# Kernel optimization log

Hardware: AMD Instinct MI355X
Metric: run time of the kernel (lower is better)

## Reference

```python
import jax, jax.numpy as jnp
import numpy as np

K_MASK = -2.3819763e38  # gemma masking constant


def apply_rope(inputs, positions, head_dim):
    # inputs: [B, T, N, H], positions: [B, T]
    half = head_dim // 2
    fraction = 2.0 * jnp.arange(half, dtype=jnp.float32) / head_dim
    timescale = 10000.0 ** fraction                      # [half]
    sinusoid = positions[..., None].astype(jnp.float32) / timescale  # [B, T, half]
    sin = jnp.sin(sinusoid)[:, :, None, :]               # [B, T, 1, half]
    cos = jnp.cos(sinusoid)[:, :, None, :]
    first, second = jnp.split(inputs, 2, axis=-1)
    out = jnp.concatenate([first * cos - second * sin,
                           second * cos + first * sin], axis=-1)
    return out.astype(inputs.dtype)


def setup_inputs() -> dict:
    key = jax.random.key(0)
    k0, k1, k2, k3 = jax.random.split(key, 4)
    B, T, D, N, H = 4, 1024, 2048, 16, 128
    x = jax.random.normal(k0, (B, T, D), dtype=jnp.float32)
    wq = jax.random.normal(k1, (N, D, H), dtype=jnp.float32) * 0.02
    wkv = jax.random.normal(k2, (2, 1, D, H), dtype=jnp.float32) * 0.02  # MQA: 1 kv head
    wo = jax.random.normal(k3, (N, H, D), dtype=jnp.float32) * 0.02
    segment_pos = jnp.broadcast_to(jnp.arange(T, dtype=jnp.int32), (B, T))
    attn_mask = jnp.broadcast_to(jnp.tril(jnp.ones((T, T), dtype=bool)), (B, T, T))
    return {"x": x, "wq": wq, "wkv": wkv, "wo": wo,
            "segment_pos": segment_pos, "attn_mask": attn_mask}


def reference(x, wq, wkv, wo, segment_pos, attn_mask):
    N, _, H = wq.shape
    # projections
    q = jnp.einsum('BTD,NDH->BTNH', x, wq)          # [B,T,N,H]
    kv = jnp.einsum('BSD,CKDH->CBSKH', x, wkv)      # [2,B,S,1,H]
    k, v = kv[0], kv[1]
    # RoPE + scaling
    q = apply_rope(q, segment_pos, H) * (H ** -0.5)
    k = apply_rope(k, segment_pos, H)
    # MQA head repeat: 1 kv head -> N heads
    k = jnp.repeat(k, N, axis=-2)                   # [B,S,N,H]
    v = jnp.repeat(v, N, axis=-2)
    # attention with manual masked softmax
    logits = jnp.einsum('BTNH,BSNH->BTNS', q, k)
    padded = jnp.where(attn_mask[:, :, None, :], logits, K_MASK)
    probs = jax.nn.softmax(padded, axis=-1).astype(k.dtype)
    encoded = jnp.einsum('BTNS,BSNH->BTNH', probs, v)
    return jnp.einsum('BTNH,NHD->BTD', encoded, wo)
```

## Files before the change

kernel.cpp:

```cpp
#include <hip/hip_runtime.h>
#include <cstdint>
#include <cstddef>

typedef unsigned short u16;
typedef __attribute__((ext_vector_type(8))) short bf16x8;
typedef __attribute__((ext_vector_type(4))) float f32x4;

#define B_ 4
#define T_ 1024
#define D_ 2048
#define N_ 16
#define H_ 128
#define BT_ (B_ * T_)
#define KMASK (-2.3819763e38f)

__device__ __forceinline__ u16 f2bf(float f) {
  uint32_t u = __builtin_bit_cast(uint32_t, f);
  u += 0x7FFFu + ((u >> 16) & 1u);
  return (u16)(u >> 16);
}
__device__ __forceinline__ float bf2f(uint32_t u) {
  return __builtin_bit_cast(float, u << 16);
}

__device__ __forceinline__ void gload16(const void* g, void* l) {
  __builtin_amdgcn_global_load_lds((const __attribute__((address_space(1))) void*)g,
                                   (__attribute__((address_space(3))) void*)l, 16, 0, 0);
}

__global__ __launch_bounds__(256) void convert_x_kernel(const float* __restrict__ x,
                                                        u16* __restrict__ xb) {
  int i = (blockIdx.x * 256 + threadIdx.x) * 8;
  float4 v0 = *(const float4*)(x + i);
  float4 v1 = *(const float4*)(x + i + 4);
  uint4 o;
  o.x = (uint32_t)f2bf(v0.x) | ((uint32_t)f2bf(v0.y) << 16);
  o.y = (uint32_t)f2bf(v0.z) | ((uint32_t)f2bf(v0.w) << 16);
  o.z = (uint32_t)f2bf(v1.x) | ((uint32_t)f2bf(v1.y) << 16);
  o.w = (uint32_t)f2bf(v1.z) | ((uint32_t)f2bf(v1.w) << 16);
  *(uint4*)(xb + i) = o;
}

__global__ __launch_bounds__(256) void transpose_kernel(const float* __restrict__ src,
                                                        u16* __restrict__ dst, int R, int C) {
  __shared__ float tile[32][33];
  const int z = blockIdx.z;
  const float* s = src + (size_t)z * R * C;
  u16* d = dst + (size_t)z * R * C;
  const int tx = threadIdx.x, ty = threadIdx.y;
  const int r0 = blockIdx.y * 32, c0 = blockIdx.x * 32;
#pragma unroll
  for (int i = 0; i < 4; ++i)
    tile[ty + i * 8][tx] = s[(size_t)(r0 + ty + i * 8) * C + (c0 + tx)];
  __syncthreads();
#pragma unroll
  for (int i = 0; i < 4; ++i)
    d[(size_t)(c0 + ty + i * 8) * R + (r0 + tx)] = f2bf(tile[tx][ty + i * 8]);
}

__global__ __launch_bounds__(256) void rope_table_kernel(float* __restrict__ costab,
                                                         float* __restrict__ sintab) {
  int idx = blockIdx.x * 256 + threadIdx.x;
  int p = idx >> 6, i = idx & 63;
  float ts = powf(10000.0f, (float)i * (1.0f / 64.0f));
  float ang = (float)p / ts;
  costab[idx] = cosf(ang);
  sintab[idx] = sinf(ang);
}

__global__ __launch_bounds__(256) void proj_gemm_kernel(
    const u16* __restrict__ xb, const u16* __restrict__ wqT, const u16* __restrict__ wkvT,
    u16* __restrict__ qraw, u16* __restrict__ kraw, u16* __restrict__ vT) {
  __shared__ alignas(16) u16 a_lds[128 * 64];
  __shared__ alignas(16) u16 b_lds[128 * 64];
  const int bid = blockIdx.x;
  const int newbid = (bid & 7) * 72 + (bid >> 3);
  const int y = newbid >> 5;
  const int m0 = (newbid & 31) * 128;
  const u16* Bt = (y < N_) ? (wqT + (size_t)y * H_ * D_) : (wkvT + (size_t)(y - N_) * H_ * D_);
  const int tid = threadIdx.x;
  const int w = tid >> 6, lane = tid & 63;
  const int g = lane >> 4, li = lane & 15;
  const int mrow = (w >> 1) * 64, wc = (w & 1) * 64;
  f32x4 acc[4][4];
#pragma unroll
  for (int i = 0; i < 4; ++i)
#pragma unroll
    for (int j = 0; j < 4; ++j) acc[i][j] = (f32x4){0.f, 0.f, 0.f, 0.f};

  for (int k0 = 0; k0 < D_; k0 += 64) {
    __syncthreads();
#pragma unroll
    for (int it = 0; it < 4; ++it) {
      int chunk = it * 256 + tid;
      int row = chunk >> 3, cu = chunk & 7;
      gload16(xb + (size_t)(m0 + row) * D_ + k0 + ((cu ^ (row & 7)) << 3), &a_lds[chunk * 8]);
    }
#pragma unroll
    for (int it = 0; it < 4; ++it) {
      int chunk = it * 256 + tid;
      int row = chunk >> 3, cu = chunk & 7;
      gload16(Bt + (size_t)row * D_ + k0 + ((cu ^ (row & 7)) << 3), &b_lds[chunk * 8]);
    }
    __syncthreads();
#pragma unroll
    for (int c2 = 0; c2 < 2; ++c2) {
      bf16x8 af[4], bfr[4];
#pragma unroll
      for (int i = 0; i < 4; ++i) {
        int row = mrow + i * 16 + li;
        af[i] = *(const bf16x8*)((const char*)a_lds +
                                 row * 128 + ((c2 * 64 + g * 16) ^ ((row & 7) << 4)));
      }
#pragma unroll
      for (int j = 0; j < 4; ++j) {
        int row = wc + j * 16 + li;
        bfr[j] = *(const bf16x8*)((const char*)b_lds +
                                  row * 128 + ((c2 * 64 + g * 16) ^ ((row & 7) << 4)));
      }
#pragma unroll
      for (int i = 0; i < 4; ++i)
#pragma unroll
        for (int j = 0; j < 4; ++j)
          acc[i][j] = __builtin_amdgcn_mfma_f32_16x16x32_bf16(af[i], bfr[j], acc[i][j], 0, 0, 0);
    }
  }

  const int b = m0 >> 10;
  if (y == N_ + 1) {
    const int tbase0 = (m0 & 1023) + mrow;
#pragma unroll
    for (int i = 0; i < 4; ++i) {
      int tbase = tbase0 + i * 16 + g * 4;
#pragma unroll
      for (int j = 0; j < 4; ++j) {
        int h = wc + j * 16 + li;
        ushort4 pk;
        pk.x = f2bf(acc[i][j][0]);
        pk.y = f2bf(acc[i][j][1]);
        pk.z = f2bf(acc[i][j][2]);
        pk.w = f2bf(acc[i][j][3]);
        *(ushort4*)(vT + ((size_t)(b * H_ + h)) * T_ + tbase) = pk;
      }
    }
  } else {
    size_t rowbase = (y < N_) ? ((size_t)(b * N_ + y) * T_ + (m0 & 1023)) : (size_t)m0;
    u16* dst0 = (y < N_) ? qraw : kraw;
#pragma unroll
    for (int i = 0; i < 4; ++i)
#pragma unroll
      for (int r = 0; r < 4; ++r) {
        int trow = mrow + i * 16 + g * 4 + r;
        u16* dst = dst0 + (rowbase + trow) * H_;
#pragma unroll
        for (int j = 0; j < 4; ++j) dst[wc + j * 16 + li] = f2bf(acc[i][j][r]);
      }
  }
}

__global__ __launch_bounds__(256) void rope_apply_k_kernel(
    const u16* __restrict__ kraw, const int* __restrict__ segment_pos,
    const float* __restrict__ costab, const float* __restrict__ sintab,
    u16* __restrict__ kb) {
  const int rid = blockIdx.x * 8 + (threadIdx.x >> 5);
  const int j = threadIdx.x & 31;
  const u16* src = kraw + (size_t)rid * H_;
  u16* dst = kb + (size_t)rid * H_;
  int p = segment_pos[rid];
  p = p < 0 ? 0 : (p > 1023 ? 1023 : p);
  uint32_t ua = *(const uint32_t*)(src + 2 * j);
  uint32_t ub = *(const uint32_t*)(src + 64 + 2 * j);
  float2 cv = *(const float2*)(costab + p * 64 + 2 * j);
  float2 sv = *(const float2*)(sintab + p * 64 + 2 * j);
  float f1a = bf2f(ua & 0xffffu), f1b = bf2f(ua >> 16);
  float f2a = bf2f(ub & 0xffffu), f2b = bf2f(ub >> 16);
  *(uint32_t*)(dst + 2 * j) =
      (uint32_t)f2bf(f1a * cv.x - f2a * sv.x) | ((uint32_t)f2bf(f1b * cv.y - f2b * sv.y) << 16);
  *(uint32_t*)(dst + 64 + 2 * j) =
      (uint32_t)f2bf(f2a * cv.x + f1a * sv.x) | ((uint32_t)f2bf(f2b * cv.y + f1b * sv.y) << 16);
}

__global__ __launch_bounds__(256) void attn_kernel(
    const u16* __restrict__ qraw, const u16* __restrict__ kb, const u16* __restrict__ vT,
    const int* __restrict__ segment_pos, const float* __restrict__ costab,
    const float* __restrict__ sintab, u16* __restrict__ enc) {
  __shared__ alignas(16) u16 k_lds[2][64 * 128];
  __shared__ alignas(16) u16 p_lds[4 * 32 * 64];
  const int bx = blockIdx.x;
  const int qt8 = 7 - (bx >> 6);
  const int bn = bx & 63;
  const int b = bn >> 4, n = bn & 15;
  const int tid = threadIdx.x, w = tid >> 6, lane = tid & 63;
  const int g = lane >> 4, li = lane & 15;
  const int t0w = qt8 * 128 + w * 32;
  char* pbase = (char*)p_lds + w * 4096;

  bf16x8 qf[2][4];
  const float scale = 0.08838834764831845f;
#pragma unroll
  for (int i = 0; i < 2; ++i) {
    const int trow = t0w + i * 16 + li;
    const u16* qrow = qraw + ((size_t)(b * N_ + n) * T_ + trow) * H_;
#pragma unroll
    for (int c = 0; c < 4; ++c) qf[i][c] = *(const bf16x8*)(qrow + c * 32 + g * 8);
    int p = segment_pos[b * T_ + trow];
    p = p < 0 ? 0 : (p > 1023 ? 1023 : p);
#pragma unroll
    for (int c = 0; c < 2; ++c) {
      const float* cp = costab + p * 64 + c * 32 + g * 8;
      const float* sp = sintab + p * 64 + c * 32 + g * 8;
      f32x4 cv0 = *(const f32x4*)cp, cv1 = *(const f32x4*)(cp + 4);
      f32x4 sv0 = *(const f32x4*)sp, sv1 = *(const f32x4*)(sp + 4);
#pragma unroll
      for (int e = 0; e < 8; ++e) {
        float cvv = e < 4 ? cv0[e] : cv1[e - 4];
        float svv = e < 4 ? sv0[e] : sv1[e - 4];
        float f1 = bf2f((u16)qf[i][c][e]);
        float f2 = bf2f((u16)qf[i][c + 2][e]);
        qf[i][c][e] = (short)f2bf((f1 * cvv - f2 * svv) * scale);
        qf[i][c + 2][e] = (short)f2bf((f2 * cvv + f1 * svv) * scale);
      }
    }
  }

  f32x4 o[2][8];
#pragma unroll
  for (int i = 0; i < 2; ++i)
#pragma unroll
    for (int hn = 0; hn < 8; ++hn) o[i][hn] = (f32x4){0.f, 0.f, 0.f, 0.f};
  float m[2] = {-3e38f, -3e38f}, lsum[2] = {0.f, 0.f};

  auto stageK = [&](int buf, int s0) {
#pragma unroll
    for (int it = 0; it < 4; ++it) {
      int chunk = it * 256 + tid;
      int row = chunk >> 4, cu = chunk & 15;
      gload16(kb + ((size_t)b * T_ + s0 + row) * H_ + ((cu ^ (row & 7)) << 3),
              &k_lds[buf][chunk * 8]);
    }
  };

  const int nst = 2 * (qt8 + 1);
  stageK(0, 0);
  __syncthreads();
  int cur = 0;
  for (int st = 0; st < nst; ++st) {
    const int s0 = st * 64;
    if (st + 1 < nst) stageK(cur ^ 1, (st + 1) * 64);
    if (s0 <= t0w + 31) {
      bf16x8 vf[2][8];
#pragma unroll
      for (int c2 = 0; c2 < 2; ++c2)
#pragma unroll
        for (int hn = 0; hn < 8; ++hn)
          vf[c2][hn] =
              *(const bf16x8*)(vT + ((size_t)(b * H_ + hn * 16 + li)) * T_ + s0 + c2 * 32 + g * 8);

      f32x4 sacc[2][4];
#pragma unroll
      for (int i = 0; i < 2; ++i)
#pragma unroll
        for (int fn = 0; fn < 4; ++fn) sacc[i][fn] = (f32x4){0.f, 0.f, 0.f, 0.f};
      __builtin_amdgcn_s_setprio(1);
#pragma unroll
      for (int c = 0; c < 4; ++c) {
        bf16x8 kf[4];
#pragma unroll
        for (int fn = 0; fn < 4; ++fn) {
          int row = fn * 16 + li;
          kf[fn] = *(const bf16x8*)((const char*)&k_lds[cur][0] +
                                    row * 256 + ((c * 64 + g * 16) ^ ((row & 7) << 4)));
        }
#pragma unroll
        for (int i = 0; i < 2; ++i)
#pragma unroll
          for (int fn = 0; fn < 4; ++fn)
            sacc[i][fn] = __builtin_amdgcn_mfma_f32_16x16x32_bf16(kf[fn], qf[i][c],
                                                                  sacc[i][fn], 0, 0, 0);
      }
      __builtin_amdgcn_s_setprio(0);

      const bool needmask = (s0 + 63 > t0w);
#pragma unroll
      for (int i = 0; i < 2; ++i) {
        if (needmask) {
          int trow = t0w + i * 16 + li;
#pragma unroll
          for (int fn = 0; fn < 4; ++fn)
#pragma unroll
            for (int r = 0; r < 4; ++r)
              if (s0 + fn * 16 + g * 4 + r > trow) sacc[i][fn][r] = KMASK;
        }
        float mx = -3e38f;
#pragma unroll
        for (int fn = 0; fn < 4; ++fn)
#pragma unroll
          for (int r = 0; r < 4; ++r) mx = fmaxf(mx, sacc[i][fn][r]);
        mx = fmaxf(mx, __shfl_xor(mx, 16, 64));
        mx = fmaxf(mx, __shfl_xor(mx, 32, 64));
        float mn = fmaxf(m[i], mx);
        float alpha = __expf(m[i] - mn);
        m[i] = mn;
        float ps = 0.f;
#pragma unroll
        for (int fn = 0; fn < 4; ++fn)
#pragma unroll
          for (int r = 0; r < 4; ++r) {
            float p = __expf(sacc[i][fn][r] - mn);
            sacc[i][fn][r] = p;
            ps += p;
          }
        ps += __shfl_xor(ps, 16, 64);
        ps += __shfl_xor(ps, 32, 64);
        lsum[i] = lsum[i] * alpha + ps;
#pragma unroll
        for (int fn = 0; fn < 4; ++fn) {
          ushort4 pk;
          pk.x = f2bf(sacc[i][fn][0]);
          pk.y = f2bf(sacc[i][fn][1]);
          pk.z = f2bf(sacc[i][fn][2]);
          pk.w = f2bf(sacc[i][fn][3]);
          *(ushort4*)(pbase + (i * 16 + li) * 128 + ((fn * 32 + g * 8) ^ ((li & 7) << 4))) = pk;
        }
#pragma unroll
        for (int r = 0; r < 4; ++r) {
          float ar = __shfl(alpha, g * 4 + r, 64);
#pragma unroll
          for (int hn = 0; hn < 8; ++hn) o[i][hn][r] *= ar;
        }
      }

      __builtin_amdgcn_s_setprio(1);
#pragma unroll
      for (int i = 0; i < 2; ++i)
#pragma unroll
        for (int c2 = 0; c2 < 2; ++c2) {
          bf16x8 pf = *(const bf16x8*)(pbase + (i * 16 + li) * 128 +
                                       ((c2 * 64 + g * 16) ^ ((li & 7) << 4)));
#pragma unroll
          for (int hn = 0; hn < 8; ++hn)
            o[i][hn] = __builtin_amdgcn_mfma_f32_16x16x32_bf16(pf, vf[c2][hn], o[i][hn], 0, 0, 0);
        }
      __builtin_amdgcn_s_setprio(0);
    }
    __syncthreads();
    cur ^= 1;
  }

#pragma unroll
  for (int i = 0; i < 2; ++i)
#pragma unroll
    for (int r = 0; r < 4; ++r) {
      float lr = __shfl(lsum[i], g * 4 + r, 64);
      float inv = 1.0f / lr;
      int t = t0w + i * 16 + g * 4 + r;
      u16* dst = enc + ((size_t)(b * T_ + t)) * (N_ * H_) + n * H_;
#pragma unroll
      for (int hn = 0; hn < 8; ++hn) dst[hn * 16 + li] = f2bf(o[i][hn][r] * inv);
    }
}

__global__ __launch_bounds__(256) void out_gemm_kernel(const u16* __restrict__ enc,
                                                       const u16* __restrict__ woT,
                                                       float* __restrict__ out) {
  __shared__ alignas(16) u16 a_lds[128 * 64];
  __shared__ alignas(16) u16 b_lds[128 * 64];
  const int bid = blockIdx.x;
  const int newbid = (bid & 7) * 64 + (bid >> 3);
  const int m0 = (newbid & 31) * 128;
  const int n0 = (newbid >> 5) * 128;
  const int tid = threadIdx.x, w = tid >> 6, lane = tid & 63;
  const int g = lane >> 4, li = lane & 15;
  const int mrow = (w >> 1) * 64, wc = (w & 1) * 64;
  f32x4 acc[4][4];
#pragma unroll
  for (int i = 0; i < 4; ++i)
#pragma unroll
    for (int j = 0; j < 4; ++j) acc[i][j] = (f32x4){0.f, 0.f, 0.f, 0.f};

  for (int k0 = 0; k0 < D_; k0 += 64) {
    __syncthreads();
#pragma unroll
    for (int it = 0; it < 4; ++it) {
      int chunk = it * 256 + tid;
      int row = chunk >> 3, cu = chunk & 7;
      gload16(enc + (size_t)(m0 + row) * D_ + k0 + ((cu ^ (row & 7)) << 3), &a_lds[chunk * 8]);
    }
#pragma unroll
    for (int it = 0; it < 4; ++it) {
      int chunk = it * 256 + tid;
      int row = chunk >> 3, cu = chunk & 7;
      gload16(woT + (size_t)(n0 + row) * D_ + k0 + ((cu ^ (row & 7)) << 3), &b_lds[chunk * 8]);
    }
    __syncthreads();
#pragma unroll
    for (int c2 = 0; c2 < 2; ++c2) {
      bf16x8 af[4], bfr[4];
#pragma unroll
      for (int i = 0; i < 4; ++i) {
        int row = mrow + i * 16 + li;
        af[i] = *(const bf16x8*)((const char*)a_lds +
                                 row * 128 + ((c2 * 64 + g * 16) ^ ((row & 7) << 4)));
      }
#pragma unroll
      for (int j = 0; j < 4; ++j) {
        int row = wc + j * 16 + li;
        bfr[j] = *(const bf16x8*)((const char*)b_lds +
                                  row * 128 + ((c2 * 64 + g * 16) ^ ((row & 7) << 4)));
      }
#pragma unroll
      for (int i = 0; i < 4; ++i)
#pragma unroll
        for (int j = 0; j < 4; ++j)
          acc[i][j] = __builtin_amdgcn_mfma_f32_16x16x32_bf16(af[i], bfr[j], acc[i][j], 0, 0, 0);
    }
  }
#pragma unroll
  for (int i = 0; i < 4; ++i)
#pragma unroll
    for (int r = 0; r < 4; ++r) {
      int bt = m0 + mrow + i * 16 + g * 4 + r;
      float* dst = out + (size_t)bt * D_ + n0 + wc;
#pragma unroll
      for (int j = 0; j < 4; ++j) dst[j * 16 + li] = acc[i][j][r];
    }
}

extern "C" void kernel_launch(void* const* d_in, const int* in_sizes, int n_in,
                              void* d_out, int out_size, void* d_ws, size_t ws_size,
                              hipStream_t stream) {
  const float* x = (const float*)d_in[0];
  const float* wq = (const float*)d_in[1];
  const float* wkv = (const float*)d_in[2];
  const float* wo = (const float*)d_in[3];
  const int* segment_pos = (const int*)d_in[4];
  float* out = (float*)d_out;

  char* ws = (char*)d_ws;
  size_t off = 0;
  auto alloc = [&](size_t bytes) -> void* {
    void* p = ws + off;
    off += (bytes + 255) & ~(size_t)255;
    return p;
  };
  u16* xb   = (u16*)alloc((size_t)BT_ * D_ * 2);
  u16* wqT  = (u16*)alloc((size_t)N_ * H_ * D_ * 2);
  u16* wkvT = (u16*)alloc((size_t)2 * H_ * D_ * 2);
  u16* woT  = (u16*)alloc((size_t)D_ * N_ * H_ * 2);
  u16* qraw = (u16*)alloc((size_t)B_ * N_ * T_ * H_ * 2);
  u16* kb   = (u16*)alloc((size_t)B_ * T_ * H_ * 2);
  u16* kraw = (u16*)alloc((size_t)B_ * T_ * H_ * 2);
  u16* vT   = (u16*)alloc((size_t)B_ * H_ * T_ * 2);
  u16* enc  = (u16*)alloc((size_t)BT_ * N_ * H_ * 2);
  float* costab = (float*)alloc(1024 * 64 * 4);
  float* sintab = (float*)alloc(1024 * 64 * 4);

  convert_x_kernel<<<BT_ * D_ / 8 / 256, 256, 0, stream>>>(x, xb);
  dim3 tb(32, 8);
  transpose_kernel<<<dim3(H_ / 32, D_ / 32, N_), tb, 0, stream>>>(wq, wqT, D_, H_);
  transpose_kernel<<<dim3(H_ / 32, D_ / 32, 2), tb, 0, stream>>>(wkv, wkvT, D_, H_);
  transpose_kernel<<<dim3(D_ / 32, D_ / 32, 1), tb, 0, stream>>>(wo, woT, N_ * H_, D_);
  rope_table_kernel<<<256, 256, 0, stream>>>(costab, sintab);
  proj_gemm_kernel<<<576, 256, 0, stream>>>(xb, wqT, wkvT, qraw, kraw, vT);
  rope_apply_k_kernel<<<BT_ / 8, 256, 0, stream>>>(kraw, segment_pos, costab, sintab, kb);
  attn_kernel<<<512, 256, 0, stream>>>(qraw, kb, vT, segment_pos, costab, sintab, enc);
  out_gemm_kernel<<<512, 256, 0, stream>>>(enc, woT, out);
}
```

Before: 211.4 us.

## Pair mirrored causal query tiles per block and stage V through LDS

Each attention block now processes two 64-row query tiles, j and 15-j, so every block walks the same number of key steps and causal work is balanced across blocks. K and V tiles for both halves are shared from LDS. V is now staged into a double-buffered swizzled LDS buffer next to K, replacing per-wave global loads of V fragments. This adds LDS use (an extra 32KB) and possible occupancy loss, and the low tile only runs its MFMAs while st<=j.

```diff
diff --git a/kernel.cpp b/kernel.cpp
--- a/kernel.cpp
+++ b/kernel.cpp
@@ -185,24 +185,24 @@
     const int* __restrict__ segment_pos, const float* __restrict__ costab,
     const float* __restrict__ sintab, u16* __restrict__ enc) {
   __shared__ alignas(16) u16 k_lds[2][64 * 128];
-  __shared__ alignas(16) u16 p_lds[4 * 32 * 64];
+  __shared__ alignas(16) u16 v_lds[2][128 * 64];
+  __shared__ alignas(16) u16 p_lds[4 * 2 * 16 * 64];
   const int bx = blockIdx.x;
-  const int qt8 = 7 - (bx >> 6);
+  const int j = bx >> 6;
   const int bn = bx & 63;
   const int b = bn >> 4, n = bn & 15;
   const int tid = threadIdx.x, w = tid >> 6, lane = tid & 63;
   const int g = lane >> 4, li = lane & 15;
-  const int t0w = qt8 * 128 + w * 32;
-  char* pbase = (char*)p_lds + w * 4096;
+  const int t0g[2] = {j * 64 + w * 16, (15 - j) * 64 + w * 16};
 
   bf16x8 qf[2][4];
   const float scale = 0.08838834764831845f;
 #pragma unroll
-  for (int i = 0; i < 2; ++i) {
-    const int trow = t0w + i * 16 + li;
+  for (int u = 0; u < 2; ++u) {
+    const int trow = t0g[u] + li;
     const u16* qrow = qraw + ((size_t)(b * N_ + n) * T_ + trow) * H_;
 #pragma unroll
-    for (int c = 0; c < 4; ++c) qf[i][c] = *(const bf16x8*)(qrow + c * 32 + g * 8);
+    for (int c = 0; c < 4; ++c) qf[u][c] = *(const bf16x8*)(qrow + c * 32 + g * 8);
     int p = segment_pos[b * T_ + trow];
     p = p < 0 ? 0 : (p > 1023 ? 1023 : p);
 #pragma unroll
@@ -215,22 +215,22 @@
       for (int e = 0; e < 8; ++e) {
         float cvv = e < 4 ? cv0[e] : cv1[e - 4];
         float svv = e < 4 ? sv0[e] : sv1[e - 4];
-        float f1 = bf2f((u16)qf[i][c][e]);
-        float f2 = bf2f((u16)qf[i][c + 2][e]);
-        qf[i][c][e] = (short)f2bf((f1 * cvv - f2 * svv) * scale);
-        qf[i][c + 2][e] = (short)f2bf((f2 * cvv + f1 * svv) * scale);
+        float f1 = bf2f((u16)qf[u][c][e]);
+        float f2 = bf2f((u16)qf[u][c + 2][e]);
+        qf[u][c][e] = (short)f2bf((f1 * cvv - f2 * svv) * scale);
+        qf[u][c + 2][e] = (short)f2bf((f2 * cvv + f1 * svv) * scale);
       }
     }
   }
 
   f32x4 o[2][8];
 #pragma unroll
-  for (int i = 0; i < 2; ++i)
-#pragma unroll
-    for (int hn = 0; hn < 8; ++hn) o[i][hn] = (f32x4){0.f, 0.f, 0.f, 0.f};
+  for (int u = 0; u < 2; ++u)
+#pragma unroll
+    for (int hn = 0; hn < 8; ++hn) o[u][hn] = (f32x4){0.f, 0.f, 0.f, 0.f};
   float m[2] = {-3e38f, -3e38f}, lsum[2] = {0.f, 0.f};
 
-  auto stageK = [&](int buf, int s0) {
+  auto stageKV = [&](int buf, int s0) {
 #pragma unroll
     for (int it = 0; it < 4; ++it) {
       int chunk = it * 256 + tid;
@@ -238,125 +238,136 @@
       gload16(kb + ((size_t)b * T_ + s0 + row) * H_ + ((cu ^ (row & 7)) << 3),
               &k_lds[buf][chunk * 8]);
     }
+#pragma unroll
+    for (int it = 0; it < 4; ++it) {
+      int chunk = it * 256 + tid;
+      int row = chunk >> 3, cu = chunk & 7;
+      gload16(vT + ((size_t)(b * H_ + row)) * T_ + s0 + ((cu ^ (row & 7)) << 3),
+              &v_lds[buf][chunk * 8]);
+    }
   };
 
-  const int nst = 2 * (qt8 + 1);
-  stageK(0, 0);
+  const int nst = 16 - j;
+  stageKV(0, 0);
   __syncthreads();
   int cur = 0;
   for (int st = 0; st < nst; ++st) {
     const int s0 = st * 64;
-    if (st + 1 < nst) stageK(cur ^ 1, (st + 1) * 64);
-    if (s0 <= t0w + 31) {
-      bf16x8 vf[2][8];
-#pragma unroll
-      for (int c2 = 0; c2 < 2; ++c2)
-#pragma unroll
-        for (int hn = 0; hn < 8; ++hn)
-          vf[c2][hn] =
-              *(const bf16x8*)(vT + ((size_t)(b * H_ + hn * 16 + li)) * T_ + s0 + c2 * 32 + g * 8);
-
-      f32x4 sacc[2][4];
-#pragma unroll
-      for (int i = 0; i < 2; ++i)
-#pragma unroll
-        for (int fn = 0; fn < 4; ++fn) sacc[i][fn] = (f32x4){0.f, 0.f, 0.f, 0.f};
-      __builtin_amdgcn_s_setprio(1);
-#pragma unroll
-      for (int c = 0; c < 4; ++c) {
-        bf16x8 kf[4];
-#pragma unroll
-        for (int fn = 0; fn < 4; ++fn) {
-          int row = fn * 16 + li;
-          kf[fn] = *(const bf16x8*)((const char*)&k_lds[cur][0] +
-                                    row * 256 + ((c * 64 + g * 16) ^ ((row & 7) << 4)));
+    if (st + 1 < nst) stageKV(cur ^ 1, (st + 1) * 64);
+    const bool actA = (st <= j);
+
+    f32x4 sacc[2][4];
+#pragma unroll
+    for (int u = 0; u < 2; ++u)
+#pragma unroll
+      for (int fn = 0; fn < 4; ++fn) sacc[u][fn] = (f32x4){0.f, 0.f, 0.f, 0.f};
+    __builtin_amdgcn_s_setprio(1);
+#pragma unroll
+    for (int c = 0; c < 4; ++c) {
+      bf16x8 kf[4];
+#pragma unroll
+      for (int fn = 0; fn < 4; ++fn) {
+        int row = fn * 16 + li;
+        kf[fn] = *(const bf16x8*)((const char*)&k_lds[cur][0] +
+                                  row * 256 + ((c * 64 + g * 16) ^ ((row & 7) << 4)));
+      }
+#pragma unroll
+      for (int fn = 0; fn < 4; ++fn)
+        sacc[1][fn] = __builtin_amdgcn_mfma_f32_16x16x32_bf16(kf[fn], qf[1][c], sacc[1][fn], 0, 0, 0);
+      if (actA)
+#pragma unroll
+        for (int fn = 0; fn < 4; ++fn)
+          sacc[0][fn] = __builtin_amdgcn_mfma_f32_16x16x32_bf16(kf[fn], qf[0][c], sacc[0][fn], 0, 0, 0);
+    }
+    __builtin_amdgcn_s_setprio(0);
+
+#pragma unroll
+    for (int u = 0; u < 2; ++u) {
+      if (u == 0 && !actA) continue;
+      const int t0 = t0g[u];
+      const bool needmask = (u == 0) ? (st == j) : (st == nst - 1);
+      if (needmask) {
+        int trow = t0 + li;
+#pragma unroll
+        for (int fn = 0; fn < 4; ++fn)
+#pragma unroll
+          for (int r = 0; r < 4; ++r)
+            if (s0 + fn * 16 + g * 4 + r > trow) sacc[u][fn][r] = KMASK;
+      }
+      float mx = -3e38f;
+#pragma unroll
+      for (int fn = 0; fn < 4; ++fn)
+#pragma unroll
+        for (int r = 0; r < 4; ++r) mx = fmaxf(mx, sacc[u][fn][r]);
+      mx = fmaxf(mx, __shfl_xor(mx, 16, 64));
+      mx = fmaxf(mx, __shfl_xor(mx, 32, 64));
+      float mn = fmaxf(m[u], mx);
+      float alpha = __expf(m[u] - mn);
+      m[u] = mn;
+      float ps = 0.f;
+#pragma unroll
+      for (int fn = 0; fn < 4; ++fn)
+#pragma unroll
+        for (int r = 0; r < 4; ++r) {
+          float p = __expf(sacc[u][fn][r] - mn);
+          sacc[u][fn][r] = p;
+          ps += p;
         }
-#pragma unroll
-        for (int i = 0; i < 2; ++i)
-#pragma unroll
-          for (int fn = 0; fn < 4; ++fn)
-            sacc[i][fn] = __builtin_amdgcn_mfma_f32_16x16x32_bf16(kf[fn], qf[i][c],
-                                                                  sacc[i][fn], 0, 0, 0);
-      }
-      __builtin_amdgcn_s_setprio(0);
-
-      const bool needmask = (s0 + 63 > t0w);
-#pragma unroll
-      for (int i = 0; i < 2; ++i) {
-        if (needmask) {
-          int trow = t0w + i * 16 + li;
-#pragma unroll
-          for (int fn = 0; fn < 4; ++fn)
-#pragma unroll
-            for (int r = 0; r < 4; ++r)
-              if (s0 + fn * 16 + g * 4 + r > trow) sacc[i][fn][r] = KMASK;
-        }
-        float mx = -3e38f;
-#pragma unroll
-        for (int fn = 0; fn < 4; ++fn)
-#pragma unroll
-          for (int r = 0; r < 4; ++r) mx = fmaxf(mx, sacc[i][fn][r]);
-        mx = fmaxf(mx, __shfl_xor(mx, 16, 64));
-        mx = fmaxf(mx, __shfl_xor(mx, 32, 64));
-        float mn = fmaxf(m[i], mx);
-        float alpha = __expf(m[i] - mn);
-        m[i] = mn;
-        float ps = 0.f;
-#pragma unroll
-        for (int fn = 0; fn < 4; ++fn)
-#pragma unroll
-          for (int r = 0; r < 4; ++r) {
-            float p = __expf(sacc[i][fn][r] - mn);
-            sacc[i][fn][r] = p;
-            ps += p;
-          }
-        ps += __shfl_xor(ps, 16, 64);
-        ps += __shfl_xor(ps, 32, 64);
-        lsum[i] = lsum[i] * alpha + ps;
-#pragma unroll
-        for (int fn = 0; fn < 4; ++fn) {
-          ushort4 pk;
-          pk.x = f2bf(sacc[i][fn][0]);
-          pk.y = f2bf(sacc[i][fn][1]);
-          pk.z = f2bf(sacc[i][fn][2]);
-          pk.w = f2bf(sacc[i][fn][3]);
-          *(ushort4*)(pbase + (i * 16 + li) * 128 + ((fn * 32 + g * 8) ^ ((li & 7) << 4))) = pk;
-        }
-#pragma unroll
-        for (int r = 0; r < 4; ++r) {
-          float ar = __shfl(alpha, g * 4 + r, 64);
-#pragma unroll
-          for (int hn = 0; hn < 8; ++hn) o[i][hn][r] *= ar;
-        }
-      }
-
-      __builtin_amdgcn_s_setprio(1);
-#pragma unroll
-      for (int i = 0; i < 2; ++i)
-#pragma unroll
-        for (int c2 = 0; c2 < 2; ++c2) {
-          bf16x8 pf = *(const bf16x8*)(pbase + (i * 16 + li) * 128 +
-                                       ((c2 * 64 + g * 16) ^ ((li & 7) << 4)));
-#pragma unroll
-          for (int hn = 0; hn < 8; ++hn)
-            o[i][hn] = __builtin_amdgcn_mfma_f32_16x16x32_bf16(pf, vf[c2][hn], o[i][hn], 0, 0, 0);
-        }
-      __builtin_amdgcn_s_setprio(0);
-    }
+      ps += __shfl_xor(ps, 16, 64);
+      ps += __shfl_xor(ps, 32, 64);
+      lsum[u] = lsum[u] * alpha + ps;
+      char* pbase = (char*)p_lds + (w * 2 + u) * 2048;
+#pragma unroll
+      for (int fn = 0; fn < 4; ++fn) {
+        ushort4 pk;
+        pk.x = f2bf(sacc[u][fn][0]);
+        pk.y = f2bf(sacc[u][fn][1]);
+        pk.z = f2bf(sacc[u][fn][2]);
+        pk.w = f2bf(sacc[u][fn][3]);
+        *(ushort4*)(pbase + li * 128 + ((fn * 32 + g * 8) ^ ((li & 7) << 4))) = pk;
+      }
+#pragma unroll
+      for (int r = 0; r < 4; ++r) {
+        float ar = __shfl(alpha, g * 4 + r, 64);
+#pragma unroll
+        for (int hn = 0; hn < 8; ++hn) o[u][hn][r] *= ar;
+      }
+    }
+
+    __builtin_amdgcn_s_setprio(1);
+#pragma unroll
+    for (int c2 = 0; c2 < 2; ++c2) {
+      bf16x8 pfB = *(const bf16x8*)((char*)p_lds + (w * 2 + 1) * 2048 + li * 128 +
+                                    ((c2 * 64 + g * 16) ^ ((li & 7) << 4)));
+      bf16x8 pfA;
+      if (actA)
+        pfA = *(const bf16x8*)((char*)p_lds + (w * 2 + 0) * 2048 + li * 128 +
+                               ((c2 * 64 + g * 16) ^ ((li & 7) << 4)));
+#pragma unroll
+      for (int hn = 0; hn < 8; ++hn) {
+        int hrow = hn * 16 + li;
+        bf16x8 vf = *(const bf16x8*)((const char*)&v_lds[cur][0] +
+                                     hrow * 128 + ((c2 * 64 + g * 16) ^ ((li & 7) << 4)));
+        o[1][hn] = __builtin_amdgcn_mfma_f32_16x16x32_bf16(pfB, vf, o[1][hn], 0, 0, 0);
+        if (actA)
+          o[0][hn] = __builtin_amdgcn_mfma_f32_16x16x32_bf16(pfA, vf, o[0][hn], 0, 0, 0);
+      }
+    }
+    __builtin_amdgcn_s_setprio(0);
     __syncthreads();
     cur ^= 1;
   }
 
 #pragma unroll
-  for (int i = 0; i < 2; ++i)
+  for (int u = 0; u < 2; ++u)
 #pragma unroll
     for (int r = 0; r < 4; ++r) {
-      float lr = __shfl(lsum[i], g * 4 + r, 64);
+      float lr = __shfl(lsum[u], g * 4 + r, 64);
       float inv = 1.0f / lr;
-      int t = t0w + i * 16 + g * 4 + r;
+      int t = t0g[u] + g * 4 + r;
       u16* dst = enc + ((size_t)(b * T_ + t)) * (N_ * H_) + n * H_;
 #pragma unroll
-      for (int hn = 0; hn < 8; ++hn) dst[hn * 16 + li] = f2bf(o[i][hn][r] * inv);
+      for (int hn = 0; hn < 8; ++hn) dst[hn * 16 + li] = f2bf(o[u][hn][r] * inv);
     }
 }
 
```

Measured after the change: 201.5 us. 4.7% less time.
